# Performance work log

Measured on AMD Instinct MI355X. Metric: run time of the kernel, lower is better.

## Reference

```python
import jax, jax.numpy as jnp
import numpy as np

D = 120
H = 8
HD = D // H
LN_EPS = 1e-5


def setup_inputs() -> dict:
    key = jax.random.key(0)
    ks = jax.random.split(key, 8)
    B, N = 16, 8192
    s = 1.0 / np.sqrt(D)
    return {
        "voxel_feat": jax.random.normal(ks[0], (B, N, D), dtype=jnp.float32),
        "cnn_feat": jax.random.normal(ks[1], (B, N, D), dtype=jnp.float32),
        "in_proj_w": jax.random.uniform(ks[2], (3 * D, D), minval=-s, maxval=s, dtype=jnp.float32),
        "in_proj_b": jnp.zeros((3 * D,), dtype=jnp.float32),
        "out_w": jax.random.uniform(ks[3], (D, D), minval=-s, maxval=s, dtype=jnp.float32),
        "out_b": jnp.zeros((D,), dtype=jnp.float32),
        "ln_gamma": jnp.ones((D,), dtype=jnp.float32),
        "ln_beta": jnp.zeros((D,), dtype=jnp.float32),
    }


def reference(voxel_feat, cnn_feat, in_proj_w, in_proj_b, out_w, out_b, ln_gamma, ln_beta):
    B, N, _ = voxel_feat.shape
    # (B, N, 2, D) -> (B*N, 2, D): each location is a 2-token sequence
    x = jnp.stack([voxel_feat, cnn_feat], axis=2).reshape(B * N, 2, D)
    # fused QKV projection (torch in_proj): x @ W^T + b
    qkv = x @ in_proj_w.T + in_proj_b                      # (BN, 2, 3D)
    q, k, v = jnp.split(qkv, 3, axis=-1)                   # each (BN, 2, D)
    # split heads: (BN, 2, H, HD) -> (BN, H, 2, HD)
    def heads(t):
        return t.reshape(B * N, 2, H, HD).transpose(0, 2, 1, 3)
    q, k, v = heads(q), heads(k), heads(v)
    scale = 1.0 / np.sqrt(HD)
    scores = jnp.einsum('bhqd,bhkd->bhqk', q, k) * scale   # (BN, H, 2, 2)
    attn = jax.nn.softmax(scores, axis=-1)
    o = jnp.einsum('bhqk,bhkd->bhqd', attn, v)             # (BN, H, 2, HD)
    o = o.transpose(0, 2, 1, 3).reshape(B * N, 2, D)
    y = o @ out_w.T + out_b                                # output projection
    # layernorm over last dim (eps = torch default 1e-5)
    mu = y.mean(axis=-1, keepdims=True)
    var = ((y - mu) ** 2).mean(axis=-1, keepdims=True)
    y = (y - mu) * jax.lax.rsqrt(var + LN_EPS) * ln_gamma + ln_beta
    # mean-pool the 2 tokens
    fused = y.mean(axis=1).reshape(B, N, D)
    return fused
```

## Files before the change

### kernel.cpp

```cpp
#include <hip/hip_runtime.h>
#include <hip/hip_bf16.h>
#include <stdint.h>

#define DD 120
#define HD 15
#define LN_EPS 1e-5f

typedef __attribute__((ext_vector_type(8))) short bf16x8;
typedef __attribute__((ext_vector_type(4))) float f32x4;

__device__ __forceinline__ unsigned short f2bf(float f) {
    return __bfloat16_as_ushort(__float2bfloat16(f));
}
__device__ __forceinline__ float bf2f(unsigned short h) {
    union { unsigned u; float f; } v; v.u = ((unsigned)h) << 16;
    return v.f;
}

__global__ void prep_weights(const float* __restrict__ w1, const float* __restrict__ w2,
                             const float* __restrict__ b1, const float* __restrict__ b2,
                             unsigned short* __restrict__ W1bp, unsigned short* __restrict__ W2bp) {
    int idx = blockIdx.x * blockDim.x + threadIdx.x;
    int stride = gridDim.x * blockDim.x;
    for (int p = idx; p < 24 * 4 * 64 * 8; p += stride) {
        int e = p & 7, lane = (p >> 3) & 63, kk = (p >> 9) & 3, t = p >> 11;
        int pos = t * 16 + (lane & 15);
        int part = pos >> 7, rem = pos & 127, h = rem >> 4, i = rem & 15;
        int k = kk * 32 + (lane >> 4) * 8 + e;
        float v = 0.f;
        if (k < DD)        { if (i < HD) v = w1[(part * DD + h * HD + i) * DD + k]; }
        else if (k == DD)  { if (i < HD) v = b1[part * DD + h * HD + i];
                             else if (part == 2 && h == 0) v = 1.0f; }
        W1bp[p] = f2bf(v);
    }
    for (int p = idx; p < 8 * 4 * 64 * 8; p += stride) {
        int e = p & 7, lane = (p >> 3) & 63, kk = (p >> 9) & 3, t = p >> 11;
        int n = t * 16 + (lane & 15);
        int kpad = kk * 32 + (lane >> 4) * 8 + e;
        int i = kpad & 15;
        int h = kpad >> 4;
        float v = 0.f;
        if (n < DD) {
            if (i < HD) v = w2[n * DD + h * HD + i];
            else if (kpad == 15) v = b2[n];
        }
        W2bp[p] = f2bf(v);
    }
}

__global__ __launch_bounds__(256, 3) void fused_attn(
    const float* __restrict__ voxel, const float* __restrict__ cnnf,
    const float* __restrict__ gamma, const float* __restrict__ beta,
    const unsigned short* __restrict__ W1bp, const unsigned short* __restrict__ W2bp,
    float* __restrict__ out)
{
    __shared__ __align__(16) char smem[32768];
    unsigned short* xs   = (unsigned short*)smem;
    unsigned short* obuf = (unsigned short*)(smem + 16384);
    float* yf = (float*)smem;

    const int tid = threadIdx.x;
    const int wave = tid >> 6, lane = tid & 63;
    const int lrow = lane & 15, lk = lane >> 4;
    const int w = wave;
    const int r7 = lrow & 7;
    const int tok0 = blockIdx.x * 64;

    bf16x8 A[2][4];
    #pragma unroll
    for (int kk = 0; kk < 4; ++kk) {
        A[0][kk] = *(const bf16x8*)(W1bp + ((size_t)(((0 * 8 + w) * 4 + kk) * 64 + lane)) * 8);
        A[1][kk] = *(const bf16x8*)(W1bp + ((size_t)(((1 * 8 + w) * 4 + kk) * 64 + lane)) * 8);
    }

    for (int i = tid; i < 64 * 30; i += 256) {
        int r = i / 30, c4 = i % 30;
        int gtok = tok0 + r;
        const float* src = ((gtok & 1) ? cnnf : voxel) + (size_t)(gtok >> 1) * DD + c4 * 4;
        float4 f = *(const float4*)src;
        ushort4 hv;
        hv.x = f2bf(f.x); hv.y = f2bf(f.y); hv.z = f2bf(f.z); hv.w = f2bf(f.w);
        int c8 = c4 >> 1, sub = (c4 & 1) * 8;
        *(ushort4*)((char*)xs + r * 256 + ((c8 ^ (r & 7)) << 4) + sub) = hv;
    }
    if (tid < 64) {
        int r = tid;
        ushort4 p0; p0.x = 0x3F80; p0.y = 0; p0.z = 0; p0.w = 0;
        ushort4 z0; z0.x = 0; z0.y = 0; z0.z = 0; z0.w = 0;
        char* base = (char*)xs + r * 256 + ((15 ^ (r & 7)) << 4);
        *(ushort4*)base = p0;
        *(ushort4*)(base + 8) = z0;
    }
    __syncthreads();

    bf16x8 bfr[4][4];
    #pragma unroll
    for (int b = 0; b < 4; ++b)
        #pragma unroll
        for (int kk = 0; kk < 4; ++kk) {
            int chunk = kk * 4 + lk;
            bfr[b][kk] = *(const bf16x8*)((const char*)xs + (b * 16 + lrow) * 256 + ((chunk ^ r7) << 4));
        }

    const float scale = 0.25819888974716112567f;
    #pragma unroll
    for (int hh = 0; hh < 2; ++hh) {
        int h = w + 4 * hh;
        f32x4 acc[3][4];
        #pragma unroll
        for (int part = 0; part < 3; ++part) {
            int u = hh * 3 + part;
            #pragma unroll
            for (int b = 0; b < 4; ++b) {
                f32x4 a = {0.f, 0.f, 0.f, 0.f};
                #pragma unroll
                for (int kk = 0; kk < 4; ++kk)
                    a = __builtin_amdgcn_mfma_f32_16x16x32_bf16(A[u & 1][kk], bfr[b][kk], a, 0, 0, 0);
                acc[part][b] = a;
            }
            if (u + 2 < 6) {
                int v = u + 2;
                int t2 = (v % 3) * 8 + (w + 4 * (v / 3));
                #pragma unroll
                for (int kk = 0; kk < 4; ++kk)
                    A[u & 1][kk] = *(const bf16x8*)(W1bp + ((size_t)((t2 * 4 + kk) * 64 + lane)) * 8);
            }
        }
        #pragma unroll
        for (int b = 0; b < 4; ++b) {
            f32x4 Q = acc[0][b], K = acc[1][b], V = acc[2][b];
            float kn0 = __shfl_xor(K[0], 1), kn1 = __shfl_xor(K[1], 1);
            float kn2 = __shfl_xor(K[2], 1), kn3 = __shfl_xor(K[3], 1);
            float ps = Q[0] * K[0] + Q[1] * K[1] + Q[2] * K[2] + Q[3] * K[3];
            float pn = Q[0] * kn0 + Q[1] * kn1 + Q[2] * kn2 + Q[3] * kn3;
            ps += __shfl_xor(ps, 16); ps += __shfl_xor(ps, 32);
            pn += __shfl_xor(pn, 16); pn += __shfl_xor(pn, 32);
            float d = (pn - ps) * scale;
            float p0 = 1.f / (1.f + __expf(d));
            float p1 = 1.f - p0;
            float o0 = p0 * V[0] + p1 * __shfl_xor(V[0], 1);
            float o1 = p0 * V[1] + p1 * __shfl_xor(V[1], 1);
            float o2 = p0 * V[2] + p1 * __shfl_xor(V[2], 1);
            float o3 = p0 * V[3] + p1 * __shfl_xor(V[3], 1);
            unsigned w0 = (unsigned)f2bf(o0) | ((unsigned)f2bf(o1) << 16);
            unsigned w1v = (unsigned)f2bf(o2) | ((unsigned)f2bf(o3) << 16);
            int chunk = 2 * h + (lk >> 1);
            *(uint2*)((char*)obuf + (b * 16 + lrow) * 256 + ((chunk ^ r7) << 4) + (lk & 1) * 8)
                = make_uint2(w0, w1v);
        }
    }

    bf16x8 A2[2][4];
    #pragma unroll
    for (int ti = 0; ti < 2; ++ti)
        #pragma unroll
        for (int kk = 0; kk < 4; ++kk)
            A2[ti][kk] = *(const bf16x8*)(W2bp + ((size_t)(((w + 4 * ti) * 4 + kk) * 64 + lane)) * 8);
    __syncthreads();

    {
        bf16x8 ofr[4][4];
        #pragma unroll
        for (int b = 0; b < 4; ++b)
            #pragma unroll
            for (int kk = 0; kk < 4; ++kk) {
                int chunk = kk * 4 + lk;
                ofr[b][kk] = *(const bf16x8*)((const char*)obuf + (b * 16 + lrow) * 256 + ((chunk ^ r7) << 4));
            }
        __syncthreads();
        #pragma unroll
        for (int ti = 0; ti < 2; ++ti) {
            int t = w + 4 * ti;
            int chunk = 4 * t + lk;
            #pragma unroll
            for (int b = 0; b < 4; ++b) {
                f32x4 a = {0.f, 0.f, 0.f, 0.f};
                #pragma unroll
                for (int kk = 0; kk < 4; ++kk)
                    a = __builtin_amdgcn_mfma_f32_16x16x32_bf16(A2[ti][kk], ofr[b][kk], a, 0, 0, 0);
                int row = b * 16 + lrow;
                *(f32x4*)((char*)yf + row * 512 + ((chunk ^ r7) << 4)) = a;
            }
        }
    }
    __syncthreads();

    {
        int locl = tid >> 3;
        int s = tid & 7;
        int r0 = 2 * locl, r1 = r0 + 1;
        auto rdf = [&](int r, int c) -> f32x4 {
            return *(const f32x4*)((const char*)yf + r * 512 + ((c ^ (r & 7)) << 4));
        };
        f32x4 v00 = rdf(r0, 2 * s),      v01 = rdf(r0, 2 * s + 1);
        f32x4 v02 = rdf(r0, 16 + 2 * s), v03 = rdf(r0, 16 + 2 * s + 1);
        f32x4 v10 = rdf(r1, 2 * s),      v11 = rdf(r1, 2 * s + 1);
        f32x4 v12 = rdf(r1, 16 + 2 * s), v13 = rdf(r1, 16 + 2 * s + 1);
        float a0[16], a1[16];
        #pragma unroll
        for (int j = 0; j < 4; ++j) {
            a0[j] = v00[j]; a0[4 + j] = v01[j]; a0[8 + j] = v02[j]; a0[12 + j] = v03[j];
            a1[j] = v10[j]; a1[4 + j] = v11[j]; a1[8 + j] = v12[j]; a1[12 + j] = v13[j];
        }
        float sum0 = 0.f, sq0 = 0.f, sum1 = 0.f, sq1 = 0.f;
        #pragma unroll
        for (int j = 0; j < 16; ++j) {
            sum0 += a0[j]; sq0 += a0[j] * a0[j];
            sum1 += a1[j]; sq1 += a1[j] * a1[j];
        }
        #pragma unroll
        for (int ww = 1; ww < 8; ww <<= 1) {
            sum0 += __shfl_xor(sum0, ww); sq0 += __shfl_xor(sq0, ww);
            sum1 += __shfl_xor(sum1, ww); sq1 += __shfl_xor(sq1, ww);
        }
        const float inv = 1.f / 120.f;
        float mu0 = sum0 * inv, mu1 = sum1 * inv;
        float var0 = sq0 * inv - mu0 * mu0, var1 = sq1 * inv - mu1 * mu1;
        float rs0 = rsqrtf(var0 + LN_EPS), rs1 = rsqrtf(var1 + LN_EPS);
        float* op = out + (size_t)(blockIdx.x * 32 + locl) * DD;
        {
            int c = 8 * s;
            #pragma unroll
            for (int q = 0; q < 2; ++q) {
                f32x4 gm = *(const f32x4*)(gamma + c + 4 * q);
                f32x4 bt = *(const f32x4*)(beta + c + 4 * q);
                float4 o4;
                float z0, z1;
                z0 = (a0[4 * q + 0] - mu0) * rs0; z1 = (a1[4 * q + 0] - mu1) * rs1;
                o4.x = 0.5f * (z0 + z1) * gm[0] + bt[0];
                z0 = (a0[4 * q + 1] - mu0) * rs0; z1 = (a1[4 * q + 1] - mu1) * rs1;
                o4.y = 0.5f * (z0 + z1) * gm[1] + bt[1];
                z0 = (a0[4 * q + 2] - mu0) * rs0; z1 = (a1[4 * q + 2] - mu1) * rs1;
                o4.z = 0.5f * (z0 + z1) * gm[2] + bt[2];
                z0 = (a0[4 * q + 3] - mu0) * rs0; z1 = (a1[4 * q + 3] - mu1) * rs1;
                o4.w = 0.5f * (z0 + z1) * gm[3] + bt[3];
                *(float4*)(op + c + 4 * q) = o4;
            }
        }
        if (s < 7) {
            int c = 64 + 8 * s;
            #pragma unroll
            for (int q = 0; q < 2; ++q) {
                f32x4 gm = *(const f32x4*)(gamma + c + 4 * q);
                f32x4 bt = *(const f32x4*)(beta + c + 4 * q);
                float4 o4;
                float z0, z1;
                z0 = (a0[8 + 4 * q + 0] - mu0) * rs0; z1 = (a1[8 + 4 * q + 0] - mu1) * rs1;
                o4.x = 0.5f * (z0 + z1) * gm[0] + bt[0];
                z0 = (a0[8 + 4 * q + 1] - mu0) * rs0; z1 = (a1[8 + 4 * q + 1] - mu1) * rs1;
                o4.y = 0.5f * (z0 + z1) * gm[1] + bt[1];
                z0 = (a0[8 + 4 * q + 2] - mu0) * rs0; z1 = (a1[8 + 4 * q + 2] - mu1) * rs1;
                o4.z = 0.5f * (z0 + z1) * gm[2] + bt[2];
                z0 = (a0[8 + 4 * q + 3] - mu0) * rs0; z1 = (a1[8 + 4 * q + 3] - mu1) * rs1;
                o4.w = 0.5f * (z0 + z1) * gm[3] + bt[3];
                *(float4*)(op + c + 4 * q) = o4;
            }
        }
    }
}

extern "C" void kernel_launch(void* const* d_in, const int* in_sizes, int n_in,
                              void* d_out, int out_size, void* d_ws, size_t ws_size,
                              hipStream_t stream) {
    const float* voxel = (const float*)d_in[0];
    const float* cnnf  = (const float*)d_in[1];
    const float* w1    = (const float*)d_in[2];
    const float* b1    = (const float*)d_in[3];
    const float* w2    = (const float*)d_in[4];
    const float* b2    = (const float*)d_in[5];
    const float* gamma = (const float*)d_in[6];
    const float* beta  = (const float*)d_in[7];
    float* out = (float*)d_out;

    unsigned short* W1bp = (unsigned short*)d_ws;
    unsigned short* W2bp = (unsigned short*)((char*)d_ws + 98304);

    int nloc = in_sizes[0] / DD;
    prep_weights<<<128, 256, 0, stream>>>(w1, w2, b1, b2, W1bp, W2bp);
    fused_attn<<<nloc / 32, 256, 0, stream>>>(voxel, cnnf, gamma, beta, W1bp, W2bp, out);
}
```

Before: 83.30 us.

## Make fused attention kernel persistent with double-buffered input prefetch

Turns the one-tile-per-block kernel into a persistent grid-stride loop capped at 768 blocks. Each block prefetches the next tile's fp32 inputs into registers while the current tile's MFMA work runs, then writes them to a second LDS buffer. The goal is to hide global load latency and cut per-block launch and weight-load overhead. In exchange it uses more LDS (48KB), more registers for the prefetched float4s, and extra barriers per iteration, which may lower occupancy.

```diff
diff --git a/kernel.cpp b/kernel.cpp
--- a/kernel.cpp
+++ b/kernel.cpp
@@ -11,10 +11,6 @@
 
 __device__ __forceinline__ unsigned short f2bf(float f) {
     return __bfloat16_as_ushort(__float2bfloat16(f));
-}
-__device__ __forceinline__ float bf2f(unsigned short h) {
-    union { unsigned u; float f; } v; v.u = ((unsigned)h) << 16;
-    return v.f;
 }
 
 __global__ void prep_weights(const float* __restrict__ w1, const float* __restrict__ w2,
@@ -52,113 +48,154 @@
     const float* __restrict__ voxel, const float* __restrict__ cnnf,
     const float* __restrict__ gamma, const float* __restrict__ beta,
     const unsigned short* __restrict__ W1bp, const unsigned short* __restrict__ W2bp,
-    float* __restrict__ out)
+    float* __restrict__ out, int ntile)
 {
-    __shared__ __align__(16) char smem[32768];
-    unsigned short* xs   = (unsigned short*)smem;
+    __shared__ __align__(16) char smem[49152];
+    unsigned short* xs0  = (unsigned short*)smem;
     unsigned short* obuf = (unsigned short*)(smem + 16384);
-    float* yf = (float*)smem;
+    unsigned short* xs1  = (unsigned short*)(smem + 32768);
 
     const int tid = threadIdx.x;
     const int wave = tid >> 6, lane = tid & 63;
     const int lrow = lane & 15, lk = lane >> 4;
     const int w = wave;
     const int r7 = lrow & 7;
-    const int tok0 = blockIdx.x * 64;
+    const float scale = 0.25819888974716112567f;
+
+    bf16x8 A2[2][4];
+    #pragma unroll
+    for (int ti = 0; ti < 2; ++ti)
+        #pragma unroll
+        for (int kk = 0; kk < 4; ++kk)
+            A2[ti][kk] = *(const bf16x8*)(W2bp + ((size_t)(((w + 4 * ti) * 4 + kk) * 64 + lane)) * 8);
 
     bf16x8 A[2][4];
     #pragma unroll
     for (int kk = 0; kk < 4; ++kk) {
-        A[0][kk] = *(const bf16x8*)(W1bp + ((size_t)(((0 * 8 + w) * 4 + kk) * 64 + lane)) * 8);
-        A[1][kk] = *(const bf16x8*)(W1bp + ((size_t)(((1 * 8 + w) * 4 + kk) * 64 + lane)) * 8);
+        A[0][kk] = *(const bf16x8*)(W1bp + ((size_t)(((w) * 4 + kk) * 64 + lane)) * 8);
+        A[1][kk] = *(const bf16x8*)(W1bp + ((size_t)(((8 + w) * 4 + kk) * 64 + lane)) * 8);
     }
 
-    for (int i = tid; i < 64 * 30; i += 256) {
-        int r = i / 30, c4 = i % 30;
-        int gtok = tok0 + r;
-        const float* src = ((gtok & 1) ? cnnf : voxel) + (size_t)(gtok >> 1) * DD + c4 * 4;
-        float4 f = *(const float4*)src;
-        ushort4 hv;
-        hv.x = f2bf(f.x); hv.y = f2bf(f.y); hv.z = f2bf(f.z); hv.w = f2bf(f.w);
-        int c8 = c4 >> 1, sub = (c4 & 1) * 8;
-        *(ushort4*)((char*)xs + r * 256 + ((c8 ^ (r & 7)) << 4) + sub) = hv;
-    }
-    if (tid < 64) {
-        int r = tid;
-        ushort4 p0; p0.x = 0x3F80; p0.y = 0; p0.z = 0; p0.w = 0;
-        ushort4 z0; z0.x = 0; z0.y = 0; z0.z = 0; z0.w = 0;
-        char* base = (char*)xs + r * 256 + ((15 ^ (r & 7)) << 4);
-        *(ushort4*)base = p0;
-        *(ushort4*)(base + 8) = z0;
-    }
+    float4 f[8];
+    int tile = blockIdx.x;
+
+    auto sload_lo = [&](int t) {
+        #pragma unroll
+        for (int jj = 0; jj < 4; ++jj) {
+            int i = tid + jj * 256;
+            int r = i / 30, c4 = i % 30;
+            int gtok = t * 64 + r;
+            const float* src = ((gtok & 1) ? cnnf : voxel) + (size_t)(gtok >> 1) * DD + c4 * 4;
+            f[jj] = *(const float4*)src;
+        }
+    };
+    auto sload_hi = [&](int t) {
+        #pragma unroll
+        for (int jj = 4; jj < 8; ++jj) {
+            int i = tid + jj * 256;
+            if (i < 1920) {
+                int r = i / 30, c4 = i % 30;
+                int gtok = t * 64 + r;
+                const float* src = ((gtok & 1) ? cnnf : voxel) + (size_t)(gtok >> 1) * DD + c4 * 4;
+                f[jj] = *(const float4*)src;
+            }
+        }
+    };
+    auto swrite = [&](unsigned short* xs) {
+        #pragma unroll
+        for (int jj = 0; jj < 8; ++jj) {
+            int i = tid + jj * 256;
+            if (jj < 4 || i < 1920) {
+                int r = i / 30, c4 = i % 30;
+                ushort4 hv;
+                hv.x = f2bf(f[jj].x); hv.y = f2bf(f[jj].y);
+                hv.z = f2bf(f[jj].z); hv.w = f2bf(f[jj].w);
+                int c8 = c4 >> 1, sub = (c4 & 1) * 8;
+                *(ushort4*)((char*)xs + r * 256 + ((c8 ^ (r & 7)) << 4) + sub) = hv;
+            }
+        }
+        if (tid < 64) {
+            int r = tid;
+            ushort4 p0; p0.x = 0x3F80; p0.y = 0; p0.z = 0; p0.w = 0;
+            ushort4 z0; z0.x = 0; z0.y = 0; z0.z = 0; z0.w = 0;
+            char* base = (char*)xs + r * 256 + ((15 ^ (r & 7)) << 4);
+            *(ushort4*)base = p0;
+            *(ushort4*)(base + 8) = z0;
+        }
+    };
+
+    sload_lo(tile); sload_hi(tile);
+    swrite(xs0);
     __syncthreads();
 
-    bf16x8 bfr[4][4];
-    #pragma unroll
-    for (int b = 0; b < 4; ++b)
-        #pragma unroll
-        for (int kk = 0; kk < 4; ++kk) {
-            int chunk = kk * 4 + lk;
-            bfr[b][kk] = *(const bf16x8*)((const char*)xs + (b * 16 + lrow) * 256 + ((chunk ^ r7) << 4));
-        }
-
-    const float scale = 0.25819888974716112567f;
-    #pragma unroll
-    for (int hh = 0; hh < 2; ++hh) {
-        int h = w + 4 * hh;
-        f32x4 acc[3][4];
-        #pragma unroll
-        for (int part = 0; part < 3; ++part) {
-            int u = hh * 3 + part;
+    for (int it = 0; tile < ntile; ++it, tile += gridDim.x) {
+        unsigned short* xs  = (it & 1) ? xs1 : xs0;
+        unsigned short* xsn = (it & 1) ? xs0 : xs1;
+        float* yf = (float*)((it & 1) ? (smem + 16384) : smem);
+        const int tnext = tile + gridDim.x;
+        const bool hn = tnext < ntile;
+
+        bf16x8 bfr[4][4];
+        #pragma unroll
+        for (int b = 0; b < 4; ++b)
+            #pragma unroll
+            for (int kk = 0; kk < 4; ++kk) {
+                int chunk = kk * 4 + lk;
+                bfr[b][kk] = *(const bf16x8*)((const char*)xs + (b * 16 + lrow) * 256 + ((chunk ^ r7) << 4));
+            }
+
+        if (hn) sload_lo(tnext);
+
+        #pragma unroll
+        for (int hh = 0; hh < 2; ++hh) {
+            int h = w + 4 * hh;
+            f32x4 acc[3][4];
+            #pragma unroll
+            for (int part = 0; part < 3; ++part) {
+                int u = hh * 3 + part;
+                #pragma unroll
+                for (int b = 0; b < 4; ++b) {
+                    f32x4 a = {0.f, 0.f, 0.f, 0.f};
+                    #pragma unroll
+                    for (int kk = 0; kk < 4; ++kk)
+                        a = __builtin_amdgcn_mfma_f32_16x16x32_bf16(A[u & 1][kk], bfr[b][kk], a, 0, 0, 0);
+                    acc[part][b] = a;
+                }
+                {
+                    int vv = (u + 2) % 6;
+                    int t2 = (vv % 3) * 8 + (w + 4 * (vv / 3));
+                    #pragma unroll
+                    for (int kk = 0; kk < 4; ++kk)
+                        A[u & 1][kk] = *(const bf16x8*)(W1bp + ((size_t)((t2 * 4 + kk) * 64 + lane)) * 8);
+                }
+            }
             #pragma unroll
             for (int b = 0; b < 4; ++b) {
-                f32x4 a = {0.f, 0.f, 0.f, 0.f};
-                #pragma unroll
-                for (int kk = 0; kk < 4; ++kk)
-                    a = __builtin_amdgcn_mfma_f32_16x16x32_bf16(A[u & 1][kk], bfr[b][kk], a, 0, 0, 0);
-                acc[part][b] = a;
-            }
-            if (u + 2 < 6) {
-                int v = u + 2;
-                int t2 = (v % 3) * 8 + (w + 4 * (v / 3));
-                #pragma unroll
-                for (int kk = 0; kk < 4; ++kk)
-                    A[u & 1][kk] = *(const bf16x8*)(W1bp + ((size_t)((t2 * 4 + kk) * 64 + lane)) * 8);
-            }
-        }
-        #pragma unroll
-        for (int b = 0; b < 4; ++b) {
-            f32x4 Q = acc[0][b], K = acc[1][b], V = acc[2][b];
-            float kn0 = __shfl_xor(K[0], 1), kn1 = __shfl_xor(K[1], 1);
-            float kn2 = __shfl_xor(K[2], 1), kn3 = __shfl_xor(K[3], 1);
-            float ps = Q[0] * K[0] + Q[1] * K[1] + Q[2] * K[2] + Q[3] * K[3];
-            float pn = Q[0] * kn0 + Q[1] * kn1 + Q[2] * kn2 + Q[3] * kn3;
-            ps += __shfl_xor(ps, 16); ps += __shfl_xor(ps, 32);
-            pn += __shfl_xor(pn, 16); pn += __shfl_xor(pn, 32);
-            float d = (pn - ps) * scale;
-            float p0 = 1.f / (1.f + __expf(d));
-            float p1 = 1.f - p0;
-            float o0 = p0 * V[0] + p1 * __shfl_xor(V[0], 1);
-            float o1 = p0 * V[1] + p1 * __shfl_xor(V[1], 1);
-            float o2 = p0 * V[2] + p1 * __shfl_xor(V[2], 1);
-            float o3 = p0 * V[3] + p1 * __shfl_xor(V[3], 1);
-            unsigned w0 = (unsigned)f2bf(o0) | ((unsigned)f2bf(o1) << 16);
-            unsigned w1v = (unsigned)f2bf(o2) | ((unsigned)f2bf(o3) << 16);
-            int chunk = 2 * h + (lk >> 1);
-            *(uint2*)((char*)obuf + (b * 16 + lrow) * 256 + ((chunk ^ r7) << 4) + (lk & 1) * 8)
-                = make_uint2(w0, w1v);
-        }
-    }
-
-    bf16x8 A2[2][4];
-    #pragma unroll
-    for (int ti = 0; ti < 2; ++ti)
-        #pragma unroll
-        for (int kk = 0; kk < 4; ++kk)
-            A2[ti][kk] = *(const bf16x8*)(W2bp + ((size_t)(((w + 4 * ti) * 4 + kk) * 64 + lane)) * 8);
-    __syncthreads();
-
-    {
+                f32x4 Q = acc[0][b], K = acc[1][b], V = acc[2][b];
+                float kn0 = __shfl_xor(K[0], 1), kn1 = __shfl_xor(K[1], 1);
+                float kn2 = __shfl_xor(K[2], 1), kn3 = __shfl_xor(K[3], 1);
+                float ps = Q[0] * K[0] + Q[1] * K[1] + Q[2] * K[2] + Q[3] * K[3];
+                float pn = Q[0] * kn0 + Q[1] * kn1 + Q[2] * kn2 + Q[3] * kn3;
+                ps += __shfl_xor(ps, 16); ps += __shfl_xor(ps, 32);
+                pn += __shfl_xor(pn, 16); pn += __shfl_xor(pn, 32);
+                float d = (pn - ps) * scale;
+                float p0 = 1.f / (1.f + __expf(d));
+                float p1 = 1.f - p0;
+                float o0 = p0 * V[0] + p1 * __shfl_xor(V[0], 1);
+                float o1 = p0 * V[1] + p1 * __shfl_xor(V[1], 1);
+                float o2 = p0 * V[2] + p1 * __shfl_xor(V[2], 1);
+                float o3 = p0 * V[3] + p1 * __shfl_xor(V[3], 1);
+                unsigned w0 = (unsigned)f2bf(o0) | ((unsigned)f2bf(o1) << 16);
+                unsigned w1v = (unsigned)f2bf(o2) | ((unsigned)f2bf(o3) << 16);
+                int chunk = 2 * h + (lk >> 1);
+                *(uint2*)((char*)obuf + (b * 16 + lrow) * 256 + ((chunk ^ r7) << 4) + (lk & 1) * 8)
+                    = make_uint2(w0, w1v);
+            }
+        }
+
+        if (hn) sload_hi(tnext);
+        __syncthreads();
+
         bf16x8 ofr[4][4];
         #pragma unroll
         for (int b = 0; b < 4; ++b)
@@ -168,6 +205,7 @@
                 ofr[b][kk] = *(const bf16x8*)((const char*)obuf + (b * 16 + lrow) * 256 + ((chunk ^ r7) << 4));
             }
         __syncthreads();
+
         #pragma unroll
         for (int ti = 0; ti < 2; ++ti) {
             int t = w + 4 * ti;
@@ -182,78 +220,79 @@
                 *(f32x4*)((char*)yf + row * 512 + ((chunk ^ r7) << 4)) = a;
             }
         }
-    }
-    __syncthreads();
-
-    {
-        int locl = tid >> 3;
-        int s = tid & 7;
-        int r0 = 2 * locl, r1 = r0 + 1;
-        auto rdf = [&](int r, int c) -> f32x4 {
-            return *(const f32x4*)((const char*)yf + r * 512 + ((c ^ (r & 7)) << 4));
-        };
-        f32x4 v00 = rdf(r0, 2 * s),      v01 = rdf(r0, 2 * s + 1);
-        f32x4 v02 = rdf(r0, 16 + 2 * s), v03 = rdf(r0, 16 + 2 * s + 1);
-        f32x4 v10 = rdf(r1, 2 * s),      v11 = rdf(r1, 2 * s + 1);
-        f32x4 v12 = rdf(r1, 16 + 2 * s), v13 = rdf(r1, 16 + 2 * s + 1);
-        float a0[16], a1[16];
-        #pragma unroll
-        for (int j = 0; j < 4; ++j) {
-            a0[j] = v00[j]; a0[4 + j] = v01[j]; a0[8 + j] = v02[j]; a0[12 + j] = v03[j];
-            a1[j] = v10[j]; a1[4 + j] = v11[j]; a1[8 + j] = v12[j]; a1[12 + j] = v13[j];
-        }
-        float sum0 = 0.f, sq0 = 0.f, sum1 = 0.f, sq1 = 0.f;
-        #pragma unroll
-        for (int j = 0; j < 16; ++j) {
-            sum0 += a0[j]; sq0 += a0[j] * a0[j];
-            sum1 += a1[j]; sq1 += a1[j] * a1[j];
-        }
-        #pragma unroll
-        for (int ww = 1; ww < 8; ww <<= 1) {
-            sum0 += __shfl_xor(sum0, ww); sq0 += __shfl_xor(sq0, ww);
-            sum1 += __shfl_xor(sum1, ww); sq1 += __shfl_xor(sq1, ww);
-        }
-        const float inv = 1.f / 120.f;
-        float mu0 = sum0 * inv, mu1 = sum1 * inv;
-        float var0 = sq0 * inv - mu0 * mu0, var1 = sq1 * inv - mu1 * mu1;
-        float rs0 = rsqrtf(var0 + LN_EPS), rs1 = rsqrtf(var1 + LN_EPS);
-        float* op = out + (size_t)(blockIdx.x * 32 + locl) * DD;
+        __syncthreads();
+
+        if (hn) swrite(xsn);
+
         {
-            int c = 8 * s;
-            #pragma unroll
-            for (int q = 0; q < 2; ++q) {
-                f32x4 gm = *(const f32x4*)(gamma + c + 4 * q);
-                f32x4 bt = *(const f32x4*)(beta + c + 4 * q);
-                float4 o4;
-                float z0, z1;
-                z0 = (a0[4 * q + 0] - mu0) * rs0; z1 = (a1[4 * q + 0] - mu1) * rs1;
-                o4.x = 0.5f * (z0 + z1) * gm[0] + bt[0];
-                z0 = (a0[4 * q + 1] - mu0) * rs0; z1 = (a1[4 * q + 1] - mu1) * rs1;
-                o4.y = 0.5f * (z0 + z1) * gm[1] + bt[1];
-                z0 = (a0[4 * q + 2] - mu0) * rs0; z1 = (a1[4 * q + 2] - mu1) * rs1;
-                o4.z = 0.5f * (z0 + z1) * gm[2] + bt[2];
-                z0 = (a0[4 * q + 3] - mu0) * rs0; z1 = (a1[4 * q + 3] - mu1) * rs1;
-                o4.w = 0.5f * (z0 + z1) * gm[3] + bt[3];
-                *(float4*)(op + c + 4 * q) = o4;
-            }
-        }
-        if (s < 7) {
-            int c = 64 + 8 * s;
-            #pragma unroll
-            for (int q = 0; q < 2; ++q) {
-                f32x4 gm = *(const f32x4*)(gamma + c + 4 * q);
-                f32x4 bt = *(const f32x4*)(beta + c + 4 * q);
-                float4 o4;
-                float z0, z1;
-                z0 = (a0[8 + 4 * q + 0] - mu0) * rs0; z1 = (a1[8 + 4 * q + 0] - mu1) * rs1;
-                o4.x = 0.5f * (z0 + z1) * gm[0] + bt[0];
-                z0 = (a0[8 + 4 * q + 1] - mu0) * rs0; z1 = (a1[8 + 4 * q + 1] - mu1) * rs1;
-                o4.y = 0.5f * (z0 + z1) * gm[1] + bt[1];
-                z0 = (a0[8 + 4 * q + 2] - mu0) * rs0; z1 = (a1[8 + 4 * q + 2] - mu1) * rs1;
-                o4.z = 0.5f * (z0 + z1) * gm[2] + bt[2];
-                z0 = (a0[8 + 4 * q + 3] - mu0) * rs0; z1 = (a1[8 + 4 * q + 3] - mu1) * rs1;
-                o4.w = 0.5f * (z0 + z1) * gm[3] + bt[3];
-                *(float4*)(op + c + 4 * q) = o4;
+            int locl = tid >> 3;
+            int s = tid & 7;
+            int r0 = 2 * locl, r1 = r0 + 1;
+            auto rdf = [&](int r, int c) -> f32x4 {
+                return *(const f32x4*)((const char*)yf + r * 512 + ((c ^ (r & 7)) << 4));
+            };
+            f32x4 v00 = rdf(r0, 2 * s),      v01 = rdf(r0, 2 * s + 1);
+            f32x4 v02 = rdf(r0, 16 + 2 * s), v03 = rdf(r0, 16 + 2 * s + 1);
+            f32x4 v10 = rdf(r1, 2 * s),      v11 = rdf(r1, 2 * s + 1);
+            f32x4 v12 = rdf(r1, 16 + 2 * s), v13 = rdf(r1, 16 + 2 * s + 1);
+            __syncthreads();
+            float a0[16], a1[16];
+            #pragma unroll
+            for (int j = 0; j < 4; ++j) {
+                a0[j] = v00[j]; a0[4 + j] = v01[j]; a0[8 + j] = v02[j]; a0[12 + j] = v03[j];
+                a1[j] = v10[j]; a1[4 + j] = v11[j]; a1[8 + j] = v12[j]; a1[12 + j] = v13[j];
+            }
+            float sum0 = 0.f, sq0 = 0.f, sum1 = 0.f, sq1 = 0.f;
+            #pragma unroll
+            for (int j = 0; j < 16; ++j) {
+                sum0 += a0[j]; sq0 += a0[j] * a0[j];
+                sum1 += a1[j]; sq1 += a1[j] * a1[j];
+            }
+            #pragma unroll
+            for (int ww = 1; ww < 8; ww <<= 1) {
+                sum0 += __shfl_xor(sum0, ww); sq0 += __shfl_xor(sq0, ww);
+                sum1 += __shfl_xor(sum1, ww); sq1 += __shfl_xor(sq1, ww);
+            }
+            const float inv = 1.f / 120.f;
+            float mu0 = sum0 * inv, mu1 = sum1 * inv;
+            float var0 = sq0 * inv - mu0 * mu0, var1 = sq1 * inv - mu1 * mu1;
+            float rs0 = rsqrtf(var0 + LN_EPS), rs1 = rsqrtf(var1 + LN_EPS);
+            float* op = out + (size_t)(tile * 32 + locl) * DD;
+            {
+                int c = 8 * s;
+                #pragma unroll
+                for (int q = 0; q < 2; ++q) {
+                    f32x4 gm = *(const f32x4*)(gamma + c + 4 * q);
+                    f32x4 bt = *(const f32x4*)(beta + c + 4 * q);
+                    float4 o4; float z0, z1;
+                    z0 = (a0[4 * q + 0] - mu0) * rs0; z1 = (a1[4 * q + 0] - mu1) * rs1;
+                    o4.x = 0.5f * (z0 + z1) * gm[0] + bt[0];
+                    z0 = (a0[4 * q + 1] - mu0) * rs0; z1 = (a1[4 * q + 1] - mu1) * rs1;
+                    o4.y = 0.5f * (z0 + z1) * gm[1] + bt[1];
+                    z0 = (a0[4 * q + 2] - mu0) * rs0; z1 = (a1[4 * q + 2] - mu1) * rs1;
+                    o4.z = 0.5f * (z0 + z1) * gm[2] + bt[2];
+                    z0 = (a0[4 * q + 3] - mu0) * rs0; z1 = (a1[4 * q + 3] - mu1) * rs1;
+                    o4.w = 0.5f * (z0 + z1) * gm[3] + bt[3];
+                    *(float4*)(op + c + 4 * q) = o4;
+                }
+            }
+            if (s < 7) {
+                int c = 64 + 8 * s;
+                #pragma unroll
+                for (int q = 0; q < 2; ++q) {
+                    f32x4 gm = *(const f32x4*)(gamma + c + 4 * q);
+                    f32x4 bt = *(const f32x4*)(beta + c + 4 * q);
+                    float4 o4; float z0, z1;
+                    z0 = (a0[8 + 4 * q + 0] - mu0) * rs0; z1 = (a1[8 + 4 * q + 0] - mu1) * rs1;
+                    o4.x = 0.5f * (z0 + z1) * gm[0] + bt[0];
+                    z0 = (a0[8 + 4 * q + 1] - mu0) * rs0; z1 = (a1[8 + 4 * q + 1] - mu1) * rs1;
+                    o4.y = 0.5f * (z0 + z1) * gm[1] + bt[1];
+                    z0 = (a0[8 + 4 * q + 2] - mu0) * rs0; z1 = (a1[8 + 4 * q + 2] - mu1) * rs1;
+                    o4.z = 0.5f * (z0 + z1) * gm[2] + bt[2];
+                    z0 = (a0[8 + 4 * q + 3] - mu0) * rs0; z1 = (a1[8 + 4 * q + 3] - mu1) * rs1;
+                    o4.w = 0.5f * (z0 + z1) * gm[3] + bt[3];
+                    *(float4*)(op + c + 4 * q) = o4;
+                }
             }
         }
     }
@@ -276,6 +315,8 @@
     unsigned short* W2bp = (unsigned short*)((char*)d_ws + 98304);
 
     int nloc = in_sizes[0] / DD;
+    int ntile = nloc / 32;
+    int grid = ntile < 768 ? ntile : 768;
     prep_weights<<<128, 256, 0, stream>>>(w1, w2, b1, b2, W1bp, W2bp);
-    fused_attn<<<nloc / 32, 256, 0, stream>>>(voxel, cnnf, gamma, beta, W1bp, W2bp, out);
+    fused_attn<<<grid, 256, 0, stream>>>(voxel, cnnf, gamma, beta, W1bp, W2bp, out, ntile);
 }
```

Result: slower. 275.8 us (+231.2%).
